# Kernel optimization log

Measured on AMD Instinct MI355X. Metric: run time of the kernel, lower is better.

Reference implementation:

```python
import jax, jax.numpy as jnp
import numpy as np

B, N, CIN, H, COUT = 256, 400, 128, 128, 16
THRESH = 0.6
EPS = 1e-5


def setup_inputs() -> dict:
    key = jax.random.key(0)
    ks = jax.random.split(key, 20)
    rn = lambda k, s, sc: jax.random.normal(k, s, jnp.float32) * sc
    inp = {
        "x": rn(ks[0], (B, N, CIN), 1.0),
        "adj": rn(ks[1], (B, N, N), 1.0),
        "edge": jax.random.randint(ks[2], (2, 4096), 0, N),  # unused (recomputed from adj in original)
        "batch": jnp.repeat(jnp.arange(B), N).reshape(B, N),  # graph ids; dense layout => mean over axis 1
        "W_adj": rn(ks[3], (N, N), 1.0 / np.sqrt(N)),
        "b_adj": rn(ks[4], (N,), 0.02),
        "W1": rn(ks[5], (CIN, H), 1.0 / np.sqrt(CIN)),
        "a_src1": rn(ks[6], (H,), 1.0 / np.sqrt(H)),
        "a_dst1": rn(ks[7], (H,), 1.0 / np.sqrt(H)),
        "b1": rn(ks[8], (H,), 0.02),
        "W2": rn(ks[9], (H, H), 1.0 / np.sqrt(H)),
        "a_src2": rn(ks[10], (H,), 1.0 / np.sqrt(H)),
        "a_dst2": rn(ks[11], (H,), 1.0 / np.sqrt(H)),
        "b2": rn(ks[12], (H,), 0.02),
        "ln_g": jnp.ones((H,), jnp.float32),
        "ln_b": jnp.zeros((H,), jnp.float32),
        "W_lin": rn(ks[13], (H, COUT), 1.0 / np.sqrt(H)),
        "b_lin": rn(ks[14], (COUT,), 0.02),
    }
    return inp


def _layer_norm(x, g, b):
    m = x.mean(-1, keepdims=True)
    v = ((x - m) ** 2).mean(-1, keepdims=True)
    return (x - m) * jax.lax.rsqrt(v + EPS) * g + b


def _gat(h, mask, W, a_src, a_dst, b):
    # PyG GATConv (1 head): edge i(src)->j(dst), softmax over incoming src nodes.
    hp = h @ W                                   # [B,N,H]
    e_src = hp @ a_src                           # [B,N]
    e_dst = hp @ a_dst                           # [B,N]
    score = jax.nn.leaky_relu(e_src[:, :, None] + e_dst[:, None, :], 0.2)  # [B,S,D]
    score = jnp.where(mask, score, jnp.finfo(score.dtype).min)
    alpha = jax.nn.softmax(score, axis=1)        # softmax over source axis per dst
    return jnp.einsum('bsd,bsh->bdh', alpha, hp) + b


def reference(x, adj, edge, batch, W_adj, b_adj, W1, a_src1, a_dst1, b1,
              W2, a_src2, a_dst2, b2, ln_g, ln_b, W_lin, b_lin):
    # adj -> Linear -> sigmoid -> detach -> threshold(0.6) -> binary edge mask
    a = jax.nn.sigmoid(adj @ W_adj + b_adj)
    mask = jax.lax.stop_gradient(a > THRESH)
    mask = mask | jnp.eye(N, dtype=bool)         # GATConv add_self_loops=True

    h = _gat(x, mask, W1, a_src1, a_dst1, b1)
    h = jax.nn.relu(_layer_norm(h, ln_g, ln_b))
    h = _gat(h, mask, W2, a_src2, a_dst2, b2)
    h = jax.nn.relu(_layer_norm(h, ln_g, ln_b))
    h = _gat(h, mask, W2, a_src2, a_dst2, b2)    # conv2 applied twice in original
    g = h.mean(axis=1)                           # global_mean_pool (dense per-graph layout)
    # dropout p=0.5 is identity in eval mode
    return g @ W_lin + b_lin                     # [B, COUT]
```

## Files before the change

kernel.cpp:

```cpp
#include <hip/hip_runtime.h>
#include <hip/hip_bf16.h>
#include <math.h>

#define NB 256
#define NN 400
#define NH 128
#define NCOUT 16
#define NNP 416
#define KP  416

static constexpr float LOGIT_THRESH = 0.40546510810816444f;
static constexpr float LN_EPS = 1e-5f;

typedef __attribute__((ext_vector_type(8))) short short8v;
typedef __attribute__((ext_vector_type(4))) float f32x4;

static __device__ __forceinline__ short f2bf_rne(float f) {
    unsigned u = __float_as_uint(f);
    unsigned r = (u + 0x7fff + ((u >> 16) & 1)) >> 16;
    return (short)r;
}
static __device__ __forceinline__ float bf2f(short s) {
    return __uint_as_float(((unsigned)(unsigned short)s) << 16);
}

static __device__ __forceinline__ unsigned pk_bf16(float a, float b) {
    __hip_bfloat162 h = __float22bfloat162_rn(make_float2(a, b));
    unsigned r;
    __builtin_memcpy(&r, &h, 4);
    return r;
}
static __device__ __forceinline__ void cvt8v(const float x[8], short8v& hv) {
    unsigned* hp = (unsigned*)&hv;
#pragma unroll
    for (int q = 0; q < 4; ++q) hp[q] = pk_bf16(x[2 * q], x[2 * q + 1]);
}

static __device__ __forceinline__ void gload16(const void* g, void* l) {
    __builtin_amdgcn_global_load_lds((const __attribute__((address_space(1))) void*)g,
                                     (__attribute__((address_space(3))) void*)l, 16, 0, 0);
}

__global__ __launch_bounds__(256) void k_wprep(const float* __restrict__ W,
                                               short* __restrict__ WtH)
{
    const int k0 = blockIdx.x * 32, d0 = blockIdx.y * 32;
    __shared__ float tile[32][33];
    const int t = threadIdx.x, cc = t & 31, rr = t >> 5;
#pragma unroll
    for (int i = 0; i < 4; ++i) {
        int k = k0 + rr + i * 8, d = d0 + cc;
        tile[rr + i * 8][cc] = (k < NN && d < NN) ? W[k * NN + d] : 0.f;
    }
    __syncthreads();
#pragma unroll
    for (int i = 0; i < 4; ++i) {
        int dr = rr + i * 8;
        int d = d0 + dr, k = k0 + cc;
        WtH[d * KP + k] = f2bf_rne(tile[cc][dr]);
    }
}

__global__ __launch_bounds__(256) void k_wprepW(const float* __restrict__ W,
                                                short* __restrict__ WTH)
{
    const int t = blockIdx.x * 256 + threadIdx.x;
    const int h = t >> 7, k = t & 127;
    WTH[h * NH + k] = f2bf_rne(W[k * NH + h]);
}

__global__ __launch_bounds__(256) void k_mask(const float* __restrict__ adj,
                                              const short* __restrict__ WtH,
                                              const float* __restrict__ badj,
                                              unsigned char* __restrict__ maskT)
{
    const int j   = blockIdx.x;
    const int xcd = j & 7;
    const int li  = j >> 3;
    const int panel  = xcd * 128 + (li >> 2);
    const int member = li & 3;
    const int b  = panel >> 2;
    const int s0 = (panel & 3) * 128;
    const int d0 = member * 128;

    const int t = threadIdx.x;
    const int lane = t & 63, w = t >> 6;
    const int wm = w >> 1, wn = w & 1;
    const int fr = lane & 15, fc = lane >> 4;

    __shared__ float As[2][128 * 32];
    __shared__ short Bhs[2][128 * 32];

    const float* adjb = adj + (long)b * NN * NN;

    long aG[4];
    int  aRow[4];
#pragma unroll
    for (int i = 0; i < 4; ++i) {
        int rloc = w * 32 + i * 8 + (lane >> 3);
        aRow[i] = rloc;
        int srow = s0 + rloc; srow = srow < NN ? srow : NN - 1;
        int c = (lane & 7) ^ (rloc & 7);
        aG[i] = (long)srow * NN + c * 4;
    }
    long bG[2];
#pragma unroll
    for (int i = 0; i < 2; ++i) {
        int rloc = w * 32 + i * 16 + (lane >> 2);
        int drow = d0 + rloc;
        int c = (lane & 3) ^ ((rloc >> 1) & 3);
        bG[i] = (long)drow * KP + c * 8;
    }

    f32x4 acc[4][4];
#pragma unroll
    for (int mi = 0; mi < 4; ++mi)
#pragma unroll
        for (int ni = 0; ni < 4; ++ni) acc[mi][ni] = (f32x4){0.f, 0.f, 0.f, 0.f};

    const int ca0 = (2 * fc) ^ (fr & 7);
    const int ca1 = (2 * fc + 1) ^ (fr & 7);
    const int cb  = fc ^ ((fr >> 1) & 3);

    #define STAGE(KT, BUF)                                                            \
    do {                                                                              \
        const int k0_ = (KT) * 32;                                                    \
        _Pragma("unroll")                                                             \
        for (int i = 0; i < 4; ++i) {                                                 \
            long gi = aG[i] + k0_;                                                    \
            if ((KT) == 12) {                                                         \
                int c = (lane & 7) ^ (aRow[i] & 7);                                   \
                if (c >= 4) gi = aG[i] - (long)c * 4;                                 \
            }                                                                         \
            gload16(adjb + gi, (char*)&As[BUF][0] + (w * 32 + i * 8) * 128);          \
        }                                                                             \
        _Pragma("unroll")                                                             \
        for (int i = 0; i < 2; ++i) {                                                 \
            gload16(WtH + bG[i] + k0_, (char*)&Bhs[BUF][0] + (w * 32 + i * 16) * 64); \
        }                                                                             \
    } while (0)

    STAGE(0, 0);
    asm volatile("s_waitcnt vmcnt(0)" ::: "memory");
    __builtin_amdgcn_s_barrier();

    int cur = 0;
    for (int kt = 0; kt < 13; ++kt) {
        __builtin_amdgcn_s_barrier();
        if (kt < 12) STAGE(kt + 1, cur ^ 1);
        if (kt < 12) asm volatile("s_waitcnt vmcnt(6)" ::: "memory");
        else         asm volatile("s_waitcnt vmcnt(0)" ::: "memory");
        __builtin_amdgcn_s_barrier();
        __builtin_amdgcn_sched_barrier(0);

        short8v ah[4], bh[4];
#pragma unroll
        for (int m = 0; m < 4; ++m) {
            const int row = wm * 64 + m * 16 + fr;
            float4 u0 = *(const float4*)((const char*)&As[cur][0] + row * 128 + ca0 * 16);
            float4 u1 = *(const float4*)((const char*)&As[cur][0] + row * 128 + ca1 * 16);
            float x[8] = {u0.x, u0.y, u0.z, u0.w, u1.x, u1.y, u1.z, u1.w};
            cvt8v(x, ah[m]);
        }
#pragma unroll
        for (int n = 0; n < 4; ++n) {
            const int row = wn * 64 + n * 16 + fr;
            bh[n] = *(const short8v*)((const char*)&Bhs[cur][0] + row * 64 + cb * 16);
        }
#pragma unroll
        for (int mi = 0; mi < 4; ++mi)
#pragma unroll
            for (int ni = 0; ni < 4; ++ni)
                acc[mi][ni] = __builtin_amdgcn_mfma_f32_16x16x32_bf16(ah[mi], bh[ni], acc[mi][ni], 0, 0, 0);
        cur ^= 1;
    }
    #undef STAGE

    unsigned char* mTb = maskT + (long)b * 32 * 52 * 128;
    const int dgbase = (d0 >> 4) + wn * 4;
    const int scbase = ((s0 + wm * 64) >> 3) + (fc >> 1);
    const int off8   = (fc & 1) * 4;
#pragma unroll
    for (int ni = 0; ni < 4; ++ni) {
        const int d = d0 + wn * 64 + ni * 16 + fr;
        if (d >= NN) continue;
        const float bv = badj[d];
#pragma unroll
        for (int mi = 0; mi < 4; ++mi) {
            const int s_cb = s0 + wm * 64 + mi * 16 + fc * 4;
            if (s_cb >= NNP) continue;
            uchar4 pk;
#pragma unroll
            for (int jj = 0; jj < 4; ++jj) {
                const int s = s_cb + jj;
                bool v = (s < NN) && ((acc[mi][ni][jj] + bv) > LOGIT_THRESH || s == d);
                ((unsigned char*)&pk)[jj] = v ? 1 : 0;
            }
            *(uchar4*)&mTb[((long)(dgbase + ni) * 52 + (scbase + mi * 2)) * 128 + fr * 8 + off8] = pk;
        }
    }
}

__global__ __launch_bounds__(256) void k_hp(const float* __restrict__ hin,
                                            const short* __restrict__ WTH,
                                            const float* __restrict__ asrc,
                                            const float* __restrict__ adst,
                                            short* __restrict__ hpT,
                                            float* __restrict__ e1sA, float* __restrict__ e2sA,
                                            float* __restrict__ e1dA, float* __restrict__ e2dA)
{
    const int b  = blockIdx.y;
    const int s0 = blockIdx.x * 128;
    const int t  = threadIdx.x;
    const int lane = t & 63, w = t >> 6;
    const int wm = w >> 1, wn = w & 1;
    const int fr = lane & 15, fc = lane >> 4;

    const float* hb = hin + (long)b * NN * NH;
    short* hpTb = hpT + (long)b * NH * NNP;

    f32x4 acc[4][4];
#pragma unroll
    for (int m = 0; m < 4; ++m)
#pragma unroll
        for (int n = 0; n < 4; ++n) acc[m][n] = (f32x4){0.f, 0.f, 0.f, 0.f};

    for (int kt = 0; kt < 4; ++kt) {
        const int k0 = kt * 32;
        short8v ah[4], bh[4];
#pragma unroll
        for (int m = 0; m < 4; ++m) {
            const int h = wm * 64 + m * 16 + fr;
            ah[m] = *(const short8v*)&WTH[h * NH + k0 + fc * 8];
        }
#pragma unroll
        for (int n = 0; n < 4; ++n) {
            const int s = s0 + wn * 64 + n * 16 + fr;
            float x[8];
            if (s < NN) {
                float4 u0 = *(const float4*)&hb[(long)s * NH + k0 + fc * 8];
                float4 u1 = *(const float4*)&hb[(long)s * NH + k0 + fc * 8 + 4];
                x[0]=u0.x; x[1]=u0.y; x[2]=u0.z; x[3]=u0.w;
                x[4]=u1.x; x[5]=u1.y; x[6]=u1.z; x[7]=u1.w;
            } else {
#pragma unroll
                for (int jj = 0; jj < 8; ++jj) x[jj] = 0.f;
            }
            cvt8v(x, bh[n]);
        }
#pragma unroll
        for (int m = 0; m < 4; ++m)
#pragma unroll
            for (int n = 0; n < 4; ++n)
                acc[m][n] = __builtin_amdgcn_mfma_f32_16x16x32_bf16(ah[m], bh[n], acc[m][n], 0, 0, 0);
    }

#pragma unroll
    for (int m = 0; m < 4; ++m) {
#pragma unroll
        for (int n = 0; n < 4; ++n) {
            const int s = s0 + wn * 64 + n * 16 + fr;
            if (s >= NNP) continue;
#pragma unroll
            for (int jj = 0; jj < 4; ++jj) {
                const int h = wm * 64 + m * 16 + fc * 4 + jj;
                hpTb[h * NNP + s] = f2bf_rne(acc[m][n][jj]);
            }
        }
    }

    __shared__ float esp[2][128], edp[2][128];
    float asv[4][4], adv[4][4];
#pragma unroll
    for (int m = 0; m < 4; ++m)
#pragma unroll
        for (int jj = 0; jj < 4; ++jj) {
            const int h = wm * 64 + m * 16 + fc * 4 + jj;
            asv[m][jj] = asrc[h];
            adv[m][jj] = adst[h];
        }
    float ps[4] = {0.f, 0.f, 0.f, 0.f}, pd[4] = {0.f, 0.f, 0.f, 0.f};
#pragma unroll
    for (int n = 0; n < 4; ++n)
#pragma unroll
        for (int m = 0; m < 4; ++m)
#pragma unroll
            for (int jj = 0; jj < 4; ++jj) {
                ps[n] += acc[m][n][jj] * asv[m][jj];
                pd[n] += acc[m][n][jj] * adv[m][jj];
            }
#pragma unroll
    for (int n = 0; n < 4; ++n) {
        ps[n] += __shfl_xor(ps[n], 16); ps[n] += __shfl_xor(ps[n], 32);
        pd[n] += __shfl_xor(pd[n], 16); pd[n] += __shfl_xor(pd[n], 32);
    }
    if (fc == 0) {
#pragma unroll
        for (int n = 0; n < 4; ++n) {
            esp[wm][wn * 64 + n * 16 + fr] = ps[n];
            edp[wm][wn * 64 + n * 16 + fr] = pd[n];
        }
    }
    __syncthreads();
    if (t < 128) {
        const int s = s0 + t;
        if (s < NNP) {
            const float es = esp[0][t] + esp[1][t];
            const float ed = edp[0][t] + edp[1][t];
            const long o = (long)b * NNP + s;
            e1sA[o] = __expf(es);       e2sA[o] = __expf(0.2f * es);
            e1dA[o] = __expf(ed);       e2dA[o] = __expf(0.2f * ed);
        }
    }
}

template<int DO_LN>
__global__ __launch_bounds__(256) void k_aggr(const unsigned char* __restrict__ maskT,
                                              const short* __restrict__ hpT,
                                              const float* __restrict__ e1sA,
                                              const float* __restrict__ e2sA,
                                              const float* __restrict__ e1dA,
                                              const float* __restrict__ e2dA,
                                              const float* __restrict__ bias,
                                              const float* __restrict__ lng,
                                              const float* __restrict__ lnb,
                                              float* __restrict__ hout)
{
    const int b  = blockIdx.y;
    const int d0 = blockIdx.x * 128;
    const int t  = threadIdx.x;
    const int lane = t & 63, w = t >> 6;
    const int fr = lane & 15, fc = lane >> 4;

    __shared__ float e1s_l[NNP], e2s_l[NNP];
    __shared__ float den_l[128];
    __shared__ float lngl[128], lnbl[128];

    for (int i = t; i < NNP; i += 256) {
        const long o = (long)b * NNP + i;
        e1s_l[i] = e1sA[o];
        e2s_l[i] = e2sA[o];
    }
    if (DO_LN && t < 128) { lngl[t] = lng[t]; lnbl[t] = lnb[t]; }

    float e1dv[2], e2dv[2];
#pragma unroll
    for (int m = 0; m < 2; ++m) {
        const int d = d0 + w * 32 + m * 16 + fr;
        const bool v = d < NN;
        const long o = (long)b * NNP + (v ? d : 0);
        e1dv[m] = v ? e1dA[o] : 0.f;
        e2dv[m] = v ? e2dA[o] : 0.f;
    }
    __syncthreads();

    f32x4 acc[2][8];
#pragma unroll
    for (int m = 0; m < 2; ++m)
#pragma unroll
        for (int n = 0; n < 8; ++n) acc[m][n] = (f32x4){0.f, 0.f, 0.f, 0.f};
    float den[2] = {0.f, 0.f};

    const unsigned char* mbase = maskT + (((long)b * 32 + (d0 >> 4) + w * 2) * 52) * 128 + fr * 8;
    const short* hTb = hpT + (long)b * NH * NNP;

    for (int kt = 0; kt < 13; ++kt) {
        const int sb = kt * 32 + fc * 8;
        short8v bf_[8];
#pragma unroll
        for (int n = 0; n < 8; ++n)
            bf_[n] = *(const short8v*)&hTb[(n * 16 + fr) * NNP + sb];
        float4 e1a = *(const float4*)&e1s_l[sb];
        float4 e1b = *(const float4*)&e1s_l[sb + 4];
        float4 e2a = *(const float4*)&e2s_l[sb];
        float4 e2b = *(const float4*)&e2s_l[sb + 4];
        float e18[8] = {e1a.x, e1a.y, e1a.z, e1a.w, e1b.x, e1b.y, e1b.z, e1b.w};
        float e28[8] = {e2a.x, e2a.y, e2a.z, e2a.w, e2b.x, e2b.y, e2b.z, e2b.w};
        const long scoff = (long)(kt * 4 + fc) * 128;
#pragma unroll
        for (int m = 0; m < 2; ++m) {
            const unsigned long long mk = *(const unsigned long long*)(mbase + (long)m * 52 * 128 + scoff);
            short8v pv;
            unsigned* pw = (unsigned*)&pv;
#pragma unroll
            for (int q = 0; q < 4; ++q) {
                float p0 = fmaxf(e18[2 * q] * e1dv[m],     e28[2 * q] * e2dv[m]);
                float p1 = fmaxf(e18[2 * q + 1] * e1dv[m], e28[2 * q + 1] * e2dv[m]);
                p0 = ((mk >> (16 * q)) & 0xffULL)     ? p0 : 0.f;
                p1 = ((mk >> (16 * q + 8)) & 0xffULL) ? p1 : 0.f;
                den[m] += p0 + p1;
                pw[q] = pk_bf16(p0, p1);
            }
#pragma unroll
            for (int n = 0; n < 8; ++n)
                acc[m][n] = __builtin_amdgcn_mfma_f32_16x16x32_bf16(pv, bf_[n], acc[m][n], 0, 0, 0);
        }
    }

#pragma unroll
    for (int m = 0; m < 2; ++m) {
        den[m] += __shfl_xor(den[m], 16);
        den[m] += __shfl_xor(den[m], 32);
    }
    if (fc == 0) {
#pragma unroll
        for (int m = 0; m < 2; ++m) den_l[w * 32 + m * 16 + fr] = den[m];
    }
    __syncthreads();

    float bvh[8], lgv[8], lbv[8];
#pragma unroll
    for (int n = 0; n < 8; ++n) {
        bvh[n] = bias[n * 16 + fr];
        if (DO_LN) { lgv[n] = lngl[n * 16 + fr]; lbv[n] = lnbl[n * 16 + fr]; }
    }

    float* hb = hout + (long)b * NN * NH;

#pragma unroll
    for (int m = 0; m < 2; ++m) {
#pragma unroll
        for (int jj = 0; jj < 4; ++jj) {
            const int dl = w * 32 + m * 16 + fc * 4 + jj;
            const int d = d0 + dl;
            const float idn = 1.f / den_l[dl];
            float v[8];
            if (DO_LN) {
                float s1 = 0.f, s2 = 0.f;
#pragma unroll
                for (int n = 0; n < 8; ++n) {
                    v[n] = acc[m][n][jj] * idn + bvh[n];
                    s1 += v[n];
                    s2 += v[n] * v[n];
                }
                s1 += __shfl_xor(s1, 1); s2 += __shfl_xor(s2, 1);
                s1 += __shfl_xor(s1, 2); s2 += __shfl_xor(s2, 2);
                s1 += __shfl_xor(s1, 4); s2 += __shfl_xor(s2, 4);
                s1 += __shfl_xor(s1, 8); s2 += __shfl_xor(s2, 8);
                const float mean = s1 * (1.f / 128.f);
                const float var  = s2 * (1.f / 128.f) - mean * mean;
                const float inv  = rsqrtf(fmaxf(var, 0.f) + LN_EPS);
                if (d < NN) {
                    float* po = hb + (long)d * NH;
#pragma unroll
                    for (int n = 0; n < 8; ++n)
                        po[n * 16 + fr] = fmaxf((v[n] - mean) * inv * lgv[n] + lbv[n], 0.f);
                }
            } else {
                if (d < NN) {
                    float* po = hb + (long)d * NH;
#pragma unroll
                    for (int n = 0; n < 8; ++n)
                        po[n * 16 + fr] = acc[m][n][jj] * idn + bvh[n];
                }
            }
        }
    }
}

__global__ __launch_bounds__(128) void k_pool_lin(const float* __restrict__ h,
                                                  const float* __restrict__ Wl,
                                                  const float* __restrict__ bl,
                                                  float* __restrict__ out)
{
    const int b = blockIdx.x;
    const int t = threadIdx.x;
    const float* hb = h + (long)b * NN * NH;
    float s = 0.f;
    for (int n = 0; n < NN; ++n) s += hb[(long)n * NH + t];
    __shared__ float gl[128];
    gl[t] = s * (1.f / NN);
    __syncthreads();
    if (t < NCOUT) {
        float o = bl[t];
        for (int k = 0; k < NH; ++k) o += gl[k] * Wl[k * NCOUT + t];
        out[b * NCOUT + t] = o;
    }
}

extern "C" void kernel_launch(void* const* d_in, const int* in_sizes, int n_in,
                              void* d_out, int out_size, void* d_ws, size_t ws_size,
                              hipStream_t stream)
{
    const float* x    = (const float*)d_in[0];
    const float* adj  = (const float*)d_in[1];
    const float* Wadj = (const float*)d_in[4];
    const float* badj = (const float*)d_in[5];
    const float* W1   = (const float*)d_in[6];
    const float* as1  = (const float*)d_in[7];
    const float* ad1  = (const float*)d_in[8];
    const float* b1   = (const float*)d_in[9];
    const float* W2   = (const float*)d_in[10];
    const float* as2  = (const float*)d_in[11];
    const float* ad2  = (const float*)d_in[12];
    const float* b2   = (const float*)d_in[13];
    const float* lng  = (const float*)d_in[14];
    const float* lnb  = (const float*)d_in[15];
    const float* Wlin = (const float*)d_in[16];
    const float* blin = (const float*)d_in[17];
    float* out = (float*)d_out;

    char* ws = (char*)d_ws;
    unsigned char* maskT = (unsigned char*)ws;
    short* hpT  = (short*)(ws + 54525952);
    float* hbuf = (float*)(ws + 81788928);
    float* e1sA = (float*)(ws + 134217728);
    float* e2sA = (float*)(ws + 134643712);
    float* e1dA = (float*)(ws + 135069696);
    float* e2dA = (float*)(ws + 135495680);
    short* WtH  = (short*)(ws + 135921664);
    short* WT1H = (short*)(ws + 136347648);
    short* WT2H = (short*)(ws + 136380416);

    k_wprep<<<dim3(13, 16), dim3(256), 0, stream>>>(Wadj, WtH);
    k_wprepW<<<dim3(64), dim3(256), 0, stream>>>(W1, WT1H);
    k_wprepW<<<dim3(64), dim3(256), 0, stream>>>(W2, WT2H);
    k_mask<<<dim3(4096), dim3(256), 0, stream>>>(adj, WtH, badj, maskT);

    k_hp<<<dim3(4, NB), dim3(256), 0, stream>>>(x, WT1H, as1, ad1, hpT,
                                                e1sA, e2sA, e1dA, e2dA);
    k_aggr<1><<<dim3(4, NB), dim3(256), 0, stream>>>(maskT, hpT, e1sA, e2sA, e1dA, e2dA,
                                                     b1, lng, lnb, hbuf);

    k_hp<<<dim3(4, NB), dim3(256), 0, stream>>>(hbuf, WT2H, as2, ad2, hpT,
                                                e1sA, e2sA, e1dA, e2dA);
    k_aggr<1><<<dim3(4, NB), dim3(256), 0, stream>>>(maskT, hpT, e1sA, e2sA, e1dA, e2dA,
                                                     b2, lng, lnb, hbuf);

    k_hp<<<dim3(4, NB), dim3(256), 0, stream>>>(hbuf, WT2H, as2, ad2, hpT,
                                                e1sA, e2sA, e1dA, e2dA);
    k_aggr<0><<<dim3(4, NB), dim3(256), 0, stream>>>(maskT, hpT, e1sA, e2sA, e1dA, e2dA,
                                                     b2, lng, lnb, hbuf);

    k_pool_lin<<<dim3(NB), dim3(128), 0, stream>>>(hbuf, Wlin, blin, out);
}
```

Baseline: 392.7 us.

## Tile hpT into 8-wide source chunks and fuse mean-pool into final aggregation

Changes the hpT layout from [H][NNP] rows to [s/8][H][8] tiles, so each MFMA B-fragment load in k_aggr reads contiguous 16-byte chunks across nearby h rows. The last aggregation no longer writes the full [B,N,H] activations. It reduces per-block node sums into a small partial buffer, and a lightweight k_pool2 finishes the mean and linear layer. This removes a large global write plus re-read in the pooling stage, at the cost of extra shuffles, a shared-memory reduction and one more sync in the final aggregation.

```diff
diff --git a/kernel.cpp b/kernel.cpp
--- a/kernel.cpp
+++ b/kernel.cpp
@@ -217,7 +217,7 @@
     const int fr = lane & 15, fc = lane >> 4;
 
     const float* hb = hin + (long)b * NN * NH;
-    short* hpTb = hpT + (long)b * NH * NNP;
+    short* hpTb = hpT + (long)b * 52 * 128 * 8;
 
     f32x4 acc[4][4];
 #pragma unroll
@@ -261,10 +261,11 @@
         for (int n = 0; n < 4; ++n) {
             const int s = s0 + wn * 64 + n * 16 + fr;
             if (s >= NNP) continue;
+            const int sc = s >> 3, so = s & 7;
 #pragma unroll
             for (int jj = 0; jj < 4; ++jj) {
                 const int h = wm * 64 + m * 16 + fc * 4 + jj;
-                hpTb[h * NNP + s] = f2bf_rne(acc[m][n][jj]);
+                hpTb[((long)sc * 128 + h) * 8 + so] = f2bf_rne(acc[m][n][jj]);
             }
         }
     }
@@ -324,10 +325,12 @@
                                               const float* __restrict__ bias,
                                               const float* __restrict__ lng,
                                               const float* __restrict__ lnb,
-                                              float* __restrict__ hout)
+                                              float* __restrict__ hout,
+                                              float* __restrict__ partial)
 {
     const int b  = blockIdx.y;
-    const int d0 = blockIdx.x * 128;
+    const int bx = blockIdx.x;
+    const int d0 = bx * 128;
     const int t  = threadIdx.x;
     const int lane = t & 63, w = t >> 6;
     const int fr = lane & 15, fc = lane >> 4;
@@ -335,6 +338,7 @@
     __shared__ float e1s_l[NNP], e2s_l[NNP];
     __shared__ float den_l[128];
     __shared__ float lngl[128], lnbl[128];
+    __shared__ float wsum[4][128];
 
     for (int i = t; i < NNP; i += 256) {
         const long o = (long)b * NNP + i;
@@ -362,14 +366,15 @@
     float den[2] = {0.f, 0.f};
 
     const unsigned char* mbase = maskT + (((long)b * 32 + (d0 >> 4) + w * 2) * 52) * 128 + fr * 8;
-    const short* hTb = hpT + (long)b * NH * NNP;
+    const short* hTb = hpT + (long)b * 52 * 128 * 8;
 
     for (int kt = 0; kt < 13; ++kt) {
         const int sb = kt * 32 + fc * 8;
+        const short* tb = hTb + (long)(kt * 4 + fc) * 128 * 8;
         short8v bf_[8];
 #pragma unroll
         for (int n = 0; n < 8; ++n)
-            bf_[n] = *(const short8v*)&hTb[(n * 16 + fr) * NNP + sb];
+            bf_[n] = *(const short8v*)&tb[(n * 16 + fr) * 8];
         float4 e1a = *(const float4*)&e1s_l[sb];
         float4 e1b = *(const float4*)&e1s_l[sb + 4];
         float4 e2a = *(const float4*)&e2s_l[sb];
@@ -417,15 +422,15 @@
 
     float* hb = hout + (long)b * NN * NH;
 
-#pragma unroll
-    for (int m = 0; m < 2; ++m) {
-#pragma unroll
-        for (int jj = 0; jj < 4; ++jj) {
-            const int dl = w * 32 + m * 16 + fc * 4 + jj;
-            const int d = d0 + dl;
-            const float idn = 1.f / den_l[dl];
-            float v[8];
-            if (DO_LN) {
+    if (DO_LN) {
+#pragma unroll
+        for (int m = 0; m < 2; ++m) {
+#pragma unroll
+            for (int jj = 0; jj < 4; ++jj) {
+                const int dl = w * 32 + m * 16 + fc * 4 + jj;
+                const int d = d0 + dl;
+                const float idn = 1.f / den_l[dl];
+                float v[8];
                 float s1 = 0.f, s2 = 0.f;
 #pragma unroll
                 for (int n = 0; n < 8; ++n) {
@@ -446,30 +451,49 @@
                     for (int n = 0; n < 8; ++n)
                         po[n * 16 + fr] = fmaxf((v[n] - mean) * inv * lgv[n] + lbv[n], 0.f);
                 }
-            } else {
-                if (d < NN) {
-                    float* po = hb + (long)d * NH;
-#pragma unroll
-                    for (int n = 0; n < 8; ++n)
-                        po[n * 16 + fr] = acc[m][n][jj] * idn + bvh[n];
-                }
-            }
-        }
-    }
-}
-
-__global__ __launch_bounds__(128) void k_pool_lin(const float* __restrict__ h,
-                                                  const float* __restrict__ Wl,
-                                                  const float* __restrict__ bl,
-                                                  float* __restrict__ out)
+            }
+        }
+    } else {
+        float psum[8] = {0.f, 0.f, 0.f, 0.f, 0.f, 0.f, 0.f, 0.f};
+#pragma unroll
+        for (int m = 0; m < 2; ++m) {
+#pragma unroll
+            for (int jj = 0; jj < 4; ++jj) {
+                const int dl = w * 32 + m * 16 + fc * 4 + jj;
+                const int d = d0 + dl;
+                if (d >= NN) continue;
+                const float idn = 1.f / den_l[dl];
+#pragma unroll
+                for (int n = 0; n < 8; ++n)
+                    psum[n] += acc[m][n][jj] * idn + bvh[n];
+            }
+        }
+#pragma unroll
+        for (int n = 0; n < 8; ++n) {
+            psum[n] += __shfl_xor(psum[n], 16);
+            psum[n] += __shfl_xor(psum[n], 32);
+        }
+        if (fc == 0) {
+#pragma unroll
+            for (int n = 0; n < 8; ++n) wsum[w][n * 16 + fr] = psum[n];
+        }
+        __syncthreads();
+        if (t < 128)
+            partial[((long)b * 4 + bx) * 128 + t] =
+                wsum[0][t] + wsum[1][t] + wsum[2][t] + wsum[3][t];
+    }
+}
+
+__global__ __launch_bounds__(128) void k_pool2(const float* __restrict__ partial,
+                                               const float* __restrict__ Wl,
+                                               const float* __restrict__ bl,
+                                               float* __restrict__ out)
 {
     const int b = blockIdx.x;
     const int t = threadIdx.x;
-    const float* hb = h + (long)b * NN * NH;
-    float s = 0.f;
-    for (int n = 0; n < NN; ++n) s += hb[(long)n * NH + t];
+    const float* pb = partial + (long)b * 4 * 128;
     __shared__ float gl[128];
-    gl[t] = s * (1.f / NN);
+    gl[t] = (pb[t] + pb[128 + t] + pb[256 + t] + pb[384 + t]) * (1.f / NN);
     __syncthreads();
     if (t < NCOUT) {
         float o = bl[t];
@@ -511,6 +535,7 @@
     short* WtH  = (short*)(ws + 135921664);
     short* WT1H = (short*)(ws + 136347648);
     short* WT2H = (short*)(ws + 136380416);
+    float* partial = (float*)(ws + 136413184);
 
     k_wprep<<<dim3(13, 16), dim3(256), 0, stream>>>(Wadj, WtH);
     k_wprepW<<<dim3(64), dim3(256), 0, stream>>>(W1, WT1H);
@@ -520,17 +545,17 @@
     k_hp<<<dim3(4, NB), dim3(256), 0, stream>>>(x, WT1H, as1, ad1, hpT,
                                                 e1sA, e2sA, e1dA, e2dA);
     k_aggr<1><<<dim3(4, NB), dim3(256), 0, stream>>>(maskT, hpT, e1sA, e2sA, e1dA, e2dA,
-                                                     b1, lng, lnb, hbuf);
+                                                     b1, lng, lnb, hbuf, partial);
 
     k_hp<<<dim3(4, NB), dim3(256), 0, stream>>>(hbuf, WT2H, as2, ad2, hpT,
                                                 e1sA, e2sA, e1dA, e2dA);
     k_aggr<1><<<dim3(4, NB), dim3(256), 0, stream>>>(maskT, hpT, e1sA, e2sA, e1dA, e2dA,
-                                                     b2, lng, lnb, hbuf);
+                                                     b2, lng, lnb, hbuf, partial);
 
     k_hp<<<dim3(4, NB), dim3(256), 0, stream>>>(hbuf, WT2H, as2, ad2, hpT,
                                                 e1sA, e2sA, e1dA, e2dA);
     k_aggr<0><<<dim3(4, NB), dim3(256), 0, stream>>>(maskT, hpT, e1sA, e2sA, e1dA, e2dA,
-                                                     b2, lng, lnb, hbuf);
-
-    k_pool_lin<<<dim3(NB), dim3(128), 0, stream>>>(hbuf, Wlin, blin, out);
-}
+                                                     b2, lng, lnb, hbuf, partial);
+
+    k_pool2<<<dim3(NB), dim3(128), 0, stream>>>(partial, Wlin, blin, out);
+}
```

New measurement: 357.6 us. 1.1x faster.
